# Kernel tuning notes

Measured on AMD Instinct MI355X. Metric: run time of the kernel, lower is better.

The kernel has to match this reference:

```python
import jax, jax.numpy as jnp
import numpy as np

B, N, EDGES = 16, 50000, 1600000
CLAMP_MIN, CLAMP_MAX = -10.0, 10.0
EPS = 1e-6


def setup_inputs() -> dict:
    key = jax.random.key(0)
    ks = jax.random.split(key, 8)
    return {
        "chem_influence": jax.random.normal(ks[0], (B, N), dtype=jnp.float32),
        "E": jax.random.normal(ks[1], (B, N), dtype=jnp.float32),
        "o_pre": jax.random.uniform(ks[2], (B, N), dtype=jnp.float32),
        "w": jax.random.normal(ks[3], (EDGES,), dtype=jnp.float32),
        "threshold": jax.random.uniform(ks[4], (N,), dtype=jnp.float32),
        "decay": jax.random.uniform(ks[5], (N,), dtype=jnp.float32),
        "src": jax.random.randint(ks[6], (EDGES,), 0, N, dtype=jnp.int32),
        "dst": jax.random.randint(ks[7], (EDGES,), 0, N, dtype=jnp.int32),
    }


def reference(chem_influence, E, o_pre, w, threshold, decay, src, dst):
    # Gap-junction currents: gather, sign-compare, weighted scatter-add.
    Oj = o_pre[:, src]                      # (B, EDGES) presynaptic outputs
    En = E[:, dst]                          # (B, EDGES) postsynaptic internal states
    sgn = jnp.where(Oj >= En, 1.0, -1.0)
    contrib = Oj * w * sgn                  # (B, EDGES)
    gj_sum = jnp.zeros_like(chem_influence).at[:, dst].add(contrib)  # (B, N)

    # Neuron dynamics (eqs 10, 11).
    S = jnp.clip(E + chem_influence + gj_sum, CLAMP_MIN, CLAMP_MAX)
    gt = S > threshold                      # broadcast (N,) over (B, N)
    mask = (~gt) & (jnp.abs(S - E) <= EPS)
    new_o = jax.nn.relu(S - threshold)
    new_e = jnp.where(gt, new_o, jnp.where(mask, E - decay, S))
    return (new_o, new_e)
```

## Files before the change

### kernel.cpp

```cpp
#include <hip/hip_runtime.h>

#define BATCH 16
#define NNODES 50000
#define NEDGES 1600000
#define BN (BATCH * NNODES)
#define CLAMP_LO -10.0f
#define CLAMP_HI 10.0f
#define EPS_V 1e-6f

#define BSZ 64
#define NBINS 782
#define CAPE 2816
#define RPT 11
#define NBLK_P 391
#define EPB 4096

__global__ __launch_bounds__(256) void prep_fused(
    const float* __restrict__ o_pre, const float* __restrict__ E,
    const int* __restrict__ src, const int* __restrict__ dst,
    const float* __restrict__ w,
    float* __restrict__ o_t, float* __restrict__ E_t,
    uint2* __restrict__ binned, int* __restrict__ gcur) {
    __shared__ int lh[NBINS];
    const int tid = threadIdx.x, bid = blockIdx.x;
    for (int i = tid; i < NBINS; i += 256) lh[i] = 0;

    const int4*   dst4 = (const int4*)dst;
    const int4*   src4 = (const int4*)src;
    const float4* w4   = (const float4*)w;
    const int e4base = bid * (EPB / 4);
    int4 d[4], s[4];
    float4 ww[4];
    bool val[4];
#pragma unroll
    for (int j = 0; j < 4; ++j) {
        int i4 = e4base + j * 256 + tid;
        val[j] = (i4 < NEDGES / 4);
        if (val[j]) { d[j] = dst4[i4]; s[j] = src4[i4]; ww[j] = w4[i4]; }
    }

    if (tid < 128) {
        int t = bid * 128 + tid;
        if (t < NNODES) {
            float v[BATCH], u[BATCH];
#pragma unroll
            for (int b = 0; b < BATCH; ++b) {
                v[b] = o_pre[b * NNODES + t];
                u[b] = E[b * NNODES + t];
            }
            float4* op = (float4*)(o_t + (size_t)t * BATCH);
            float4* ep = (float4*)(E_t + (size_t)t * BATCH);
#pragma unroll
            for (int k = 0; k < 4; ++k) {
                op[k] = make_float4(v[4*k], v[4*k+1], v[4*k+2], v[4*k+3]);
                ep[k] = make_float4(u[4*k], u[4*k+1], u[4*k+2], u[4*k+3]);
            }
        }
    }
    __syncthreads();

#pragma unroll
    for (int j = 0; j < 4; ++j) {
        if (val[j]) {
            atomicAdd(&lh[d[j].x >> 6], 1);
            atomicAdd(&lh[d[j].y >> 6], 1);
            atomicAdd(&lh[d[j].z >> 6], 1);
            atomicAdd(&lh[d[j].w >> 6], 1);
        }
    }
    __syncthreads();

    for (int i = tid; i < NBINS; i += 256) {
        int c = lh[i];
        int base = c ? atomicAdd(&gcur[i], c) : 0;
        lh[i] = i * CAPE + base;
    }
    __syncthreads();

#pragma unroll
    for (int j = 0; j < 4; ++j) {
        if (val[j]) {
            int   dd[4] = {d[j].x, d[j].y, d[j].z, d[j].w};
            int   ss[4] = {s[j].x, s[j].y, s[j].z, s[j].w};
            float wv[4] = {ww[j].x, ww[j].y, ww[j].z, ww[j].w};
#pragma unroll
            for (int m = 0; m < 4; ++m) {
                int dn  = dd[m];
                int bin = dn >> 6;
                int pos = atomicAdd(&lh[bin], 1);
                if (pos < (bin + 1) * CAPE)
                    binned[pos] = make_uint2(
                        (unsigned)ss[m] | ((unsigned)(dn & 63) << 16),
                        __float_as_uint(wv[m]));
            }
        }
    }
}

__global__ __launch_bounds__(256, 4) void bin_gather9(
    const float* __restrict__ o_t, const float* __restrict__ E_t,
    const float* __restrict__ chem, const float* __restrict__ threshold,
    const float* __restrict__ decay, const int* __restrict__ gcur,
    const uint2* __restrict__ binned,
    float* __restrict__ out_o, float* __restrict__ out_e) {
    __shared__ int   cnt_l[BSZ];
    __shared__ int   offs[BSZ + 1];
    __shared__ uint2 eb[CAPE];
    const int k = blockIdx.x, tid = threadIdx.x;
    const int node0 = k * BSZ;
    const int nn = (NNODES - node0 < BSZ) ? (NNODES - node0) : BSZ;
    const int s0 = k * CAPE;
    int cnt = gcur[k];
    if (cnt > CAPE) cnt = CAPE;

    uint2 r[RPT];
    if (tid < BSZ) cnt_l[tid] = 0;
    __syncthreads();
#pragma unroll
    for (int j = 0; j < RPT; ++j) {
        int idx = tid + j * 256;
        if (idx < cnt) {
            uint2 p = binned[s0 + idx];
            r[j] = p;
            atomicAdd(&cnt_l[(p.x >> 16) & 63], 1);
        }
    }
    __syncthreads();

    if (tid < BSZ) {
        int c = cnt_l[tid];
        int v = c;
#pragma unroll
        for (int o = 1; o < BSZ; o <<= 1) {
            int u = __shfl_up(v, o);
            if (tid >= o) v += u;
        }
        offs[tid]  = v - c;
        cnt_l[tid] = v - c;
        if (tid == BSZ - 1) offs[BSZ] = cnt;
    }
    __syncthreads();

#pragma unroll
    for (int j = 0; j < RPT; ++j) {
        int idx = tid + j * 256;
        if (idx < cnt) {
            uint2 p = r[j];
            int pos = atomicAdd(&cnt_l[(p.x >> 16) & 63], 1);
            eb[pos] = p;
        }
    }
    __syncthreads();

    if (tid < nn * 4) {
        const int n  = tid >> 2;
        const int q4 = (tid & 3) * 4;
        const int gn = node0 + n;
        const int e0 = offs[n], e1 = offs[n + 1];
        const float4 en = *(const float4*)(E_t + (size_t)gn * BATCH + q4);
        const float th = threshold[gn];
        const float dc = decay[gn];
        float ch[4];
#pragma unroll
        for (int j = 0; j < 4; ++j) ch[j] = chem[(q4 + j) * NNODES + gn];

        float4 acc = make_float4(0.f, 0.f, 0.f, 0.f);
#define OJ(P) (*(const float4*)(o_t + (size_t)((P).x & 0xFFFFu) * BATCH + q4))
#define ACCP(OJV, P)                                                            \
        {                                                                       \
            float wv = __uint_as_float((P).y), nwv = -wv;                       \
            acc.x = fmaf((OJV).x, ((OJV).x >= en.x) ? wv : nwv, acc.x);         \
            acc.y = fmaf((OJV).y, ((OJV).y >= en.y) ? wv : nwv, acc.y);         \
            acc.z = fmaf((OJV).z, ((OJV).z >= en.z) ? wv : nwv, acc.z);         \
            acc.w = fmaf((OJV).w, ((OJV).w >= en.w) ? wv : nwv, acc.w);         \
        }
        int i = e0;
        uint2 p0, p1;
        float4 o0, o1;
        bool staged = false;
        if (i + 2 <= e1) {
            p0 = eb[i]; p1 = eb[i + 1];
            o0 = OJ(p0); o1 = OJ(p1);
            i += 2;
            staged = true;
        }
        for (; i + 2 <= e1; i += 2) {
            uint2 q0 = eb[i], q1 = eb[i + 1];
            float4 n0 = OJ(q0), n1 = OJ(q1);
            ACCP(o0, p0); ACCP(o1, p1);
            p0 = q0; p1 = q1; o0 = n0; o1 = n1;
        }
        if (staged) { ACCP(o0, p0); ACCP(o1, p1); }
        if (i < e1) {
            uint2 pt = eb[i];
            float4 ot = OJ(pt);
            ACCP(ot, pt);
        }
#undef ACCP
#undef OJ

        float ev[4] = {en.x, en.y, en.z, en.w};
        float av[4] = {acc.x, acc.y, acc.z, acc.w};
#pragma unroll
        for (int j = 0; j < 4; ++j) {
            float e = ev[j];
            float S = e + ch[j] + av[j];
            S = fminf(fmaxf(S, CLAMP_LO), CLAMP_HI);
            float no = fmaxf(S - th, 0.0f);
            float ne;
            if (S > th) ne = no;
            else if (fabsf(S - e) <= EPS_V) ne = e - dc;
            else ne = S;
            out_o[(q4 + j) * NNODES + gn] = no;
            out_e[(q4 + j) * NNODES + gn] = ne;
        }
    }
}

__global__ void edge_scatter_dev(const float* __restrict__ o_pre, const float* __restrict__ E,
                                 const float* __restrict__ w, const int* __restrict__ src,
                                 const int* __restrict__ dst, float* __restrict__ gj) {
    int e = blockIdx.x * blockDim.x + threadIdx.x;
    if (e >= NEDGES) return;
    int s = src[e];
    int d = dst[e];
    float wv = w[e];
#pragma unroll
    for (int b = 0; b < BATCH; ++b) {
        float oj = o_pre[b * NNODES + s];
        float en = E[b * NNODES + d];
        atomicAdd(&gj[b * NNODES + d], (oj >= en) ? oj * wv : -oj * wv);
    }
}

__global__ void finalize_dev(const float* __restrict__ chem, const float* __restrict__ E,
                             const float* __restrict__ threshold, const float* __restrict__ decay,
                             float* __restrict__ out_o, float* __restrict__ out_e_gj) {
    int i = blockIdx.x * blockDim.x + threadIdx.x;
    if (i >= BN) return;
    int n = i % NNODES;
    float e = E[i];
    float S = e + chem[i] + out_e_gj[i];
    S = fminf(fmaxf(S, CLAMP_LO), CLAMP_HI);
    float th = threshold[n];
    float no = fmaxf(S - th, 0.0f);
    float ne;
    if (S > th) ne = no;
    else if (fabsf(S - e) <= EPS_V) ne = e - decay[n];
    else ne = S;
    out_o[i] = no;
    out_e_gj[i] = ne;
}

extern "C" void kernel_launch(void* const* d_in, const int* in_sizes, int n_in,
                              void* d_out, int out_size, void* d_ws, size_t ws_size,
                              hipStream_t stream) {
    const float* chem      = (const float*)d_in[0];
    const float* E         = (const float*)d_in[1];
    const float* o_pre     = (const float*)d_in[2];
    const float* w         = (const float*)d_in[3];
    const float* threshold = (const float*)d_in[4];
    const float* decay     = (const float*)d_in[5];
    const int*   src       = (const int*)d_in[6];
    const int*   dst       = (const int*)d_in[7];

    float* out_o = (float*)d_out;
    float* out_e = (float*)d_out + BN;

    const size_t OT_OFF  = 0;
    const size_t ET_OFF  = 3203072;
    const size_t BIN_OFF = 6406144;
    const size_t GC_OFF  = 24023040;
    const size_t need    = GC_OFF + (size_t)NBINS * sizeof(int);

    if (ws_size >= need) {
        char* ws = (char*)d_ws;
        float* o_t    = (float*)(ws + OT_OFF);
        float* E_t    = (float*)(ws + ET_OFF);
        uint2* binned = (uint2*)(ws + BIN_OFF);
        int*   gcur   = (int*)(ws + GC_OFF);

        hipMemsetAsync(gcur, 0, (size_t)NBINS * sizeof(int), stream);
        prep_fused<<<NBLK_P, 256, 0, stream>>>(o_pre, E, src, dst, w, o_t, E_t, binned, gcur);
        bin_gather9<<<NBINS, 256, 0, stream>>>(o_t, E_t, chem, threshold, decay,
                                               gcur, binned, out_o, out_e);
    } else {
        hipMemsetAsync(out_e, 0, (size_t)BN * sizeof(float), stream);
        edge_scatter_dev<<<(NEDGES + 255) / 256, 256, 0, stream>>>(o_pre, E, w, src, dst, out_e);
        finalize_dev<<<(BN + 255) / 256, 256, 0, stream>>>(chem, E, threshold, decay, out_o, out_e);
    }
}
```

Before: 123.9 us.

## Spread prep across 512 blocks and split node transpose across all threads

Raises the prep kernel grid from 391 to 512 blocks with fewer edges per block, so work fills the device more evenly. The o_pre/E transpose now uses all 256 threads per block, each handling half of the batch for one node, instead of 128 threads doing all 16 batches. The transpose also moves to after the histogram/global-reservation step, so its latency can overlap the atomics. The trade-off is more blocks, each doing its own global bin reservation atomics, and a different edge ordering within bins.

```diff
diff --git a/kernel.cpp b/kernel.cpp
--- a/kernel.cpp
+++ b/kernel.cpp
@@ -12,8 +12,10 @@
 #define NBINS 782
 #define CAPE 2816
 #define RPT 11
-#define NBLK_P 391
-#define EPB 4096
+#define NBLK_P 512
+#define EPB 3200
+#define E4PB 800
+#define NE4 (NEDGES / 4)
 
 __global__ __launch_bounds__(256) void prep_fused(
     const float* __restrict__ o_pre, const float* __restrict__ E,
@@ -28,34 +30,16 @@
     const int4*   dst4 = (const int4*)dst;
     const int4*   src4 = (const int4*)src;
     const float4* w4   = (const float4*)w;
-    const int e4base = bid * (EPB / 4);
+    const int e4base = bid * E4PB;
+    const int e4end  = (e4base + E4PB < NE4) ? (e4base + E4PB) : NE4;
     int4 d[4], s[4];
     float4 ww[4];
     bool val[4];
 #pragma unroll
     for (int j = 0; j < 4; ++j) {
         int i4 = e4base + j * 256 + tid;
-        val[j] = (i4 < NEDGES / 4);
+        val[j] = (i4 < e4end);
         if (val[j]) { d[j] = dst4[i4]; s[j] = src4[i4]; ww[j] = w4[i4]; }
-    }
-
-    if (tid < 128) {
-        int t = bid * 128 + tid;
-        if (t < NNODES) {
-            float v[BATCH], u[BATCH];
-#pragma unroll
-            for (int b = 0; b < BATCH; ++b) {
-                v[b] = o_pre[b * NNODES + t];
-                u[b] = E[b * NNODES + t];
-            }
-            float4* op = (float4*)(o_t + (size_t)t * BATCH);
-            float4* ep = (float4*)(E_t + (size_t)t * BATCH);
-#pragma unroll
-            for (int k = 0; k < 4; ++k) {
-                op[k] = make_float4(v[4*k], v[4*k+1], v[4*k+2], v[4*k+3]);
-                ep[k] = make_float4(u[4*k], u[4*k+1], u[4*k+2], u[4*k+3]);
-            }
-        }
     }
     __syncthreads();
 
@@ -74,6 +58,26 @@
         int c = lh[i];
         int base = c ? atomicAdd(&gcur[i], c) : 0;
         lh[i] = i * CAPE + base;
+    }
+
+    {
+        int task = bid * 256 + tid;
+        int t = task >> 1;
+        int h = (task & 1) * 8;
+        if (t < NNODES) {
+            float v[8], u[8];
+#pragma unroll
+            for (int j = 0; j < 8; ++j) {
+                v[j] = o_pre[(h + j) * NNODES + t];
+                u[j] = E[(h + j) * NNODES + t];
+            }
+            float4* op = (float4*)(o_t + (size_t)t * BATCH + h);
+            float4* ep = (float4*)(E_t + (size_t)t * BATCH + h);
+            op[0] = make_float4(v[0], v[1], v[2], v[3]);
+            op[1] = make_float4(v[4], v[5], v[6], v[7]);
+            ep[0] = make_float4(u[0], u[1], u[2], u[3]);
+            ep[1] = make_float4(u[4], u[5], u[6], u[7]);
+        }
     }
     __syncthreads();
 
```

New measurement: 133.6 us. 7.8% more time.
